# Optimization experiments

Measured on AMD Instinct MI355X. Metric: run time of the kernel, lower is better.

Reference implementation:

```python
import jax, jax.numpy as jnp
import numpy as np

N, E, IN, OUT, R, B = 20000, 640000, 128, 128, 65, 65
BN_EPS = 1e-5


def setup_inputs() -> dict:
    key = jax.random.key(0)
    ks = jax.random.split(key, 8)
    node_feats = jax.random.normal(ks[0], (N, IN), dtype=jnp.float32)
    src = jax.random.randint(ks[1], (E,), 0, N, dtype=jnp.int32)
    dst = jax.random.randint(ks[2], (E,), 0, N, dtype=jnp.int32)
    etype = jax.random.randint(ks[3], (E,), 0, R, dtype=jnp.int32)
    norm = jax.random.uniform(ks[4], (E, 1), dtype=jnp.float32)
    basis = jax.random.normal(ks[5], (B, IN, OUT), dtype=jnp.float32) * 0.05
    comp = jax.random.normal(ks[6], (R, B), dtype=jnp.float32) * 0.1
    h_bias = jnp.zeros((OUT,), dtype=jnp.float32)
    W_res = jax.random.normal(ks[7], (IN, OUT), dtype=jnp.float32) * 0.05
    b_res = jnp.zeros((OUT,), dtype=jnp.float32)
    gamma = jnp.ones((OUT,), dtype=jnp.float32)
    beta = jnp.zeros((OUT,), dtype=jnp.float32)
    return dict(node_feats=node_feats, src=src, dst=dst, etype=etype, norm=norm,
                basis=basis, comp=comp, h_bias=h_bias, W_res=W_res, b_res=b_res,
                gamma=gamma, beta=beta)


def reference(node_feats, src, dst, etype, norm, basis, comp, h_bias, W_res, b_res, gamma, beta):
    n, in_f = node_feats.shape
    r = comp.shape[0]
    # Basis decomposition: W_r = sum_b comp[r,b] * basis[b]  -> (R, in, out)
    W = jnp.einsum('rb,bio->rio', comp, basis)
    # Per-edge message x[src] * norm (norm is scalar per edge so it commutes
    # with the relation matmul). Aggregate per (dst, relation) first, then do
    # one dense relation-batched GEMM (mathematically identical to DGL's
    # per-edge transform + scatter-add, since everything is linear).
    msg = node_feats[src] * norm                       # (E, in)
    seg = dst.astype(jnp.int32) * r + etype            # combined (dst, rel) key
    S = jax.ops.segment_sum(msg, seg, num_segments=n * r).reshape(n, r, in_f)
    h = jnp.einsum('nri,rio->no', S, W) + h_bias       # (N, out)
    h = jax.nn.relu(h)                                 # conv activation (dropout p=0)
    # Residual branch: relu(Linear(x))
    h = h + jax.nn.relu(node_feats @ W_res + b_res)
    # BatchNorm1d (training mode: batch stats, biased variance)
    mean = jnp.mean(h, axis=0)
    var = jnp.var(h, axis=0)
    h = (h - mean) * jax.lax.rsqrt(var + BN_EPS) * gamma + beta
    return h
```

## Files before the change

kernel.cpp:

```cpp
#include <hip/hip_runtime.h>
#include <hip/hip_bf16.h>


#define N_NODES 20000
#define E_EDGES 640000
#define R_REL   65
#define NG5     40
#define NG128   157
#define NSLOT   (NG5 * R_REL * 4)
#define NKEY5   (NG5 * R_REL)
#define NB_RESID 313
#define MAX_TILES 10240
#define TM      128

typedef __attribute__((ext_vector_type(8))) short bf16x8;
typedef __attribute__((ext_vector_type(4))) float f32x4;
typedef __attribute__((ext_vector_type(4))) unsigned int u32x4;
typedef __attribute__((ext_vector_type(2))) unsigned int u32x2;

__device__ __forceinline__ unsigned short f2bf(float x) {
    union { float f; unsigned int u; } c; c.f = x;
    unsigned int b = c.u + 0x7fffu + ((c.u >> 16) & 1u);
    return (unsigned short)(b >> 16);
}
__device__ __forceinline__ float bf2f_lo(unsigned int u) {
    union { unsigned int u; float f; } c; c.u = u << 16; return c.f;
}
__device__ __forceinline__ float bf2f_hi(unsigned int u) {
    union { unsigned int u; float f; } c; c.u = u & 0xffff0000u; return c.f;
}
__device__ __forceinline__ void async16(const void* g, void* l) {
    __builtin_amdgcn_global_load_lds(
        (const __attribute__((address_space(1))) unsigned int*)g,
        (__attribute__((address_space(3))) unsigned int*)l, 16, 0, 0);
}
__device__ __forceinline__ int unperm(int p) {
    return (p & 64) + ((p & 3) << 4) + ((p >> 2) & 15);
}

__global__ void k_prep1(const float* __restrict__ comp, const float* __restrict__ basis,
                        float* __restrict__ W32, const int* __restrict__ et,
                        const int* __restrict__ dstA, int* __restrict__ gh3,
                        int* __restrict__ gh2, const float* __restrict__ node_feats,
                        unsigned short* __restrict__ node_bf) {
    __shared__ int shbuf[15200];
    int b = blockIdx.x, t = threadIdx.x;
    if (b < 320) {
        float* lc = (float*)shbuf;
        int r0 = (b >> 6) * 16;
        int col = (b & 63) * 256 + t;
        for (int j = t; j < 16 * 65; j += 256) {
            int rr = r0 + j / 65;
            lc[j] = (rr < R_REL) ? comp[rr * 65 + (j % 65)] : 0.f;
        }
        __syncthreads();
        float acc[16];
#pragma unroll
        for (int j = 0; j < 16; ++j) acc[j] = 0.f;
        for (int k = 0; k < 65; ++k) {
            float v = basis[k * 16384 + col];
#pragma unroll
            for (int j = 0; j < 16; ++j) acc[j] += lc[j * 65 + k] * v;
        }
#pragma unroll
        for (int j = 0; j < 16; ++j) {
            int rr = r0 + j;
            if (rr < R_REL) W32[rr * 16384 + col] = acc[j];
        }
    } else if (b < 384) {
        int* pk2 = shbuf;
        int* pk3 = shbuf + 10000;
        for (int i = t; i < 15200; i += 256) shbuf[i] = 0;
        __syncthreads();
        for (int i = (b - 320) * 256 + t; i < E_EDGES; i += 64 * 256) {
            int d = dstA[i];
            int slot = ((d >> 9) * 65 + et[i]) * 4 + ((d >> 7) & 3);
            atomicAdd(&pk2[d >> 1], (int)(1u << ((d & 1) << 4)));
            atomicAdd(&pk3[slot >> 1], (int)(1u << ((slot & 1) << 4)));
        }
        __syncthreads();
        for (int i = t; i < 10000; i += 256) {
            unsigned v = (unsigned)pk2[i];
            if (v & 0xffffu) atomicAdd(&gh2[2 * i], (int)(v & 0xffffu));
            if (v >> 16)     atomicAdd(&gh2[2 * i + 1], (int)(v >> 16));
        }
        for (int i = t; i < 5200; i += 256) {
            unsigned v = (unsigned)pk3[i];
            if (v & 0xffffu) atomicAdd(&gh3[2 * i], (int)(v & 0xffffu));
            if (v >> 16)     atomicAdd(&gh3[2 * i + 1], (int)(v >> 16));
        }
    } else {
        int i = (b - 384) * 256 + t;
        if (i < N_NODES * 32) {
            float4 v = reinterpret_cast<const float4*>(node_feats)[i];
            __hip_bfloat162 b0 = __float22bfloat162_rn(make_float2(v.x, v.y));
            __hip_bfloat162 b1 = __float22bfloat162_rn(make_float2(v.z, v.w));
            u32x2 pk;
            pk.x = *reinterpret_cast<unsigned int*>(&b0);
            pk.y = *reinterpret_cast<unsigned int*>(&b1);
            reinterpret_cast<u32x2*>(node_bf)[i] = pk;
        }
    }
}

__global__ void k_prep3(const int* __restrict__ gh3, int* __restrict__ segAll,
                        const int* __restrict__ gh2, int* __restrict__ seg,
                        const float* __restrict__ W32, unsigned short* __restrict__ Wt,
                        const float* __restrict__ Wresf, unsigned short* __restrict__ Wrest) {
    int b = blockIdx.x, t = threadIdx.x;
    if (b < 41) {
        __shared__ int red[256];
        __shared__ int pref;
        int acc = 0;
        for (int i = t; i < b * 256; i += 256) acc += gh3[i];
        red[t] = acc;
        __syncthreads();
        for (int off = 128; off > 0; off >>= 1) {
            if (t < off) red[t] += red[t + off];
            __syncthreads();
        }
        if (t == 0) pref = red[0];
        __syncthreads();
        int i = b * 256 + t;
        int v = (i < NSLOT) ? gh3[i] : 0;
        red[t] = v;
        __syncthreads();
        for (int off = 1; off < 256; off <<= 1) {
            int x = (t >= off) ? red[t - off] : 0;
            __syncthreads();
            red[t] += x;
            __syncthreads();
        }
        int excl = red[t] - v + pref;
        if (i < NSLOT) {
            segAll[i] = excl;
            if (i == NSLOT - 1) segAll[NSLOT] = excl + v;
        }
    } else if (b < 120) {
        __shared__ int red[256];
        __shared__ int pref;
        int b2 = b - 41;
        int acc = 0;
        for (int i = t; i < b2 * 256; i += 256) acc += gh2[i];
        red[t] = acc;
        __syncthreads();
        for (int off = 128; off > 0; off >>= 1) {
            if (t < off) red[t] += red[t + off];
            __syncthreads();
        }
        if (t == 0) pref = red[0];
        __syncthreads();
        int i = b2 * 256 + t;
        int v = (i < N_NODES) ? gh2[i] : 0;
        red[t] = v;
        __syncthreads();
        for (int off = 1; off < 256; off <<= 1) {
            int x = (t >= off) ? red[t - off] : 0;
            __syncthreads();
            red[t] += x;
            __syncthreads();
        }
        int excl = red[t] - v + pref;
        if (i < N_NODES) {
            seg[i] = excl;
            if (i == N_NODES - 1) seg[N_NODES] = excl + v;
        }
    } else {
        __shared__ float tile[64][65];
        int bb = b - 120;
        const float* s; unsigned short* d; int sub;
        if (bb < R_REL * 4) { s = W32 + (size_t)(bb >> 2) * 16384; d = Wt + (size_t)(bb >> 2) * 16384; sub = bb & 3; }
        else { s = Wresf; d = Wrest; sub = bb - R_REL * 4; }
        int ot = (sub >> 1) & 1, itl = sub & 1;
        int tx = t & 63, ty = t >> 6;
        for (int it = 0; it < 16; ++it) {
            int i = ty + it * 4;
            tile[i][tx] = s[(itl * 64 + i) * 128 + ot * 64 + tx];
        }
        __syncthreads();
        for (int it = 0; it < 16; ++it) {
            int o = ty + it * 4;
            d[(ot * 64 + o) * 128 + itl * 64 + tx] = f2bf(tile[tx][o]);
        }
    }
}

__global__ void k_scatterA(const int* __restrict__ et, const int* __restrict__ srcA,
                           const int* __restrict__ dstA, const float* __restrict__ norm,
                           const int* __restrict__ seg, int* __restrict__ cntA,
                           u32x2* __restrict__ ebuf) {
    __shared__ int lh[NG128], lbase[NG128];
    int c0 = blockIdx.x * 2560;
    int cend = min(c0 + 2560, E_EDGES);
    int t = threadIdx.x;
    for (int i = t; i < NG128; i += 256) lh[i] = 0;
    __syncthreads();
    for (int i = c0 + t; i < cend; i += 256) atomicAdd(&lh[dstA[i] >> 7], 1);
    __syncthreads();
    for (int i = t; i < NG128; i += 256)
        if (lh[i] > 0) lbase[i] = seg[i * 128] + atomicAdd(&cntA[i], lh[i]);
    __syncthreads();
    for (int i = t; i < NG128; i += 256) lh[i] = 0;
    __syncthreads();
    for (int i = c0 + t; i < cend; i += 256) {
        int d = dstA[i];
        int g = d >> 7;
        int p = lbase[g] + atomicAdd(&lh[g], 1);
        u32x2 e;
        e.x = (unsigned)srcA[i] | ((unsigned)(d & 127) << 15) | ((unsigned)et[i] << 22);
        e.y = __float_as_uint(norm[i]);
        ebuf[p] = e;
    }
}

__global__ void k_scatterB(const u32x2* __restrict__ ebuf, const int* __restrict__ seg,
                           const int* __restrict__ segAll, int* __restrict__ srcp,
                           float* __restrict__ normp, int* __restrict__ eidx,
                           int* __restrict__ ntiles_p, int* __restrict__ tile_r,
                           int* __restrict__ tile_start, int* __restrict__ tile_len) {
    int b = blockIdx.x, t = threadIdx.x;
    if (b < NG128) {
        __shared__ int base65[R_REL], lcnt[R_REL], sdst[128], ldst[128];
        int g5 = b >> 2, sub = b & 3;
        if (t < R_REL) { base65[t] = segAll[(g5 * 65 + t) * 4 + sub]; lcnt[t] = 0; }
        if (t < 128) {
            int d = b * 128 + t;
            sdst[t] = seg[min(d, N_NODES)];
            ldst[t] = 0;
        }
        __syncthreads();
        int e0 = seg[b * 128];
        int e1 = seg[min((b + 1) * 128, N_NODES)];
        for (int i = e0 + t; i < e1; i += 1024) {
            u32x2 e = ebuf[i];
            int src = e.x & 0x7fff;
            int slot = (e.x >> 15) & 127;
            int rel = e.x >> 22;
            int p = base65[rel] + atomicAdd(&lcnt[rel], 1);
            srcp[p] = src;
            normp[p] = __uint_as_float(e.y);
            int pos = sdst[slot] + atomicAdd(&ldst[slot], 1);
            eidx[pos] = p;
        }
    } else {
        int k2 = (b - NG128) * 1024 + t;
        if (k2 < NKEY5) {
            int s = segAll[k2 * 4], e = segAll[k2 * 4 + 4];
            int len = e - s;
            if (len > 0) {
                int nt = (len + TM - 1) / TM;
                int base = atomicAdd(ntiles_p, nt);
                for (int k = 0; k < nt; ++k) {
                    tile_r[base + k] = k2 % 65;
                    tile_start[base + k] = s + k * TM;
                    tile_len[base + k] = min(TM, len - k * TM);
                }
            }
        }
    }
}

__global__ __launch_bounds__(256, 3) void k_conv_gemm(
    const int* __restrict__ tile_r, const int* __restrict__ tile_start,
    const int* __restrict__ tile_len, const int* __restrict__ ntiles_p,
    const int* __restrict__ srcp, const float* __restrict__ normp,
    const unsigned short* __restrict__ node_bf,
    const unsigned short* __restrict__ Wt, const unsigned short* __restrict__ Wrest,
    const float* __restrict__ b_res, unsigned short* __restrict__ t_out,
    float* __restrict__ resid) {
    __shared__ unsigned short Blds[128 * 128];
    __shared__ float snorm[128];
    int t = threadIdx.x;
    int w = t >> 6, lane = t & 63;
    int lrow = lane & 15, quad = lane >> 4;

    if (blockIdx.x < NB_RESID) {
        int wr = (w >> 1) * 32, wc = (w & 1) * 64;
        int row0 = blockIdx.x * 64;
        int nrows = min(64, N_NODES - row0);
        int r0i = wr + lrow, r1i = wr + 16 + lrow;
        const bf16x8* a0p = reinterpret_cast<const bf16x8*>(
            node_bf + (size_t)(row0 + ((r0i < nrows) ? r0i : 0)) * 128);
        const bf16x8* a1p = reinterpret_cast<const bf16x8*>(
            node_bf + (size_t)(row0 + ((r1i < nrows) ? r1i : 0)) * 128);
        bf16x8 areg[2][4];
#pragma unroll
        for (int ks = 0; ks < 4; ++ks) {
            int cq = ks * 4 + quad;
            areg[0][ks] = a0p[cq];
            areg[1][ks] = a1p[cq];
        }
#pragma unroll
        for (int it = 0; it < 8; ++it) {
            int j = t + 256 * it;
            int o = j >> 4, c = j & 15, cs = c ^ (o & 15);
            async16(Wrest + o * 128 + cs * 8, &Blds[o * 128 + c * 8]);
        }
        __syncthreads();
        f32x4 acc[2][4];
#pragma unroll
        for (int i = 0; i < 2; ++i)
#pragma unroll
            for (int j = 0; j < 4; ++j) acc[i][j] = (f32x4){0.f, 0.f, 0.f, 0.f};
#pragma unroll
        for (int ks = 0; ks < 4; ++ks) {
            int cs = (ks * 4 + quad) ^ lrow;
            bf16x8 bfr[4];
#pragma unroll
            for (int j = 0; j < 4; ++j)
                bfr[j] = *reinterpret_cast<const bf16x8*>(&Blds[(wc + j * 16 + lrow) * 128 + cs * 8]);
#pragma unroll
            for (int i = 0; i < 2; ++i)
#pragma unroll
                for (int j = 0; j < 4; ++j)
                    acc[i][j] = __builtin_amdgcn_mfma_f32_16x16x32_bf16(areg[i][ks], bfr[j], acc[i][j], 0, 0, 0);
        }
        float br0 = b_res[wc + lrow];
        float br1 = b_res[wc + 16 + lrow];
        float br2 = b_res[wc + 32 + lrow];
        float br3 = b_res[wc + 48 + lrow];
#pragma unroll
        for (int i = 0; i < 2; ++i) {
#pragma unroll
            for (int reg = 0; reg < 4; ++reg) {
                int grow = row0 + wr + i * 16 + quad * 4 + reg;
                if (grow < N_NODES) {
                    float4 v;
                    v.x = fmaxf(acc[i][0][reg] + br0, 0.f);
                    v.y = fmaxf(acc[i][1][reg] + br1, 0.f);
                    v.z = fmaxf(acc[i][2][reg] + br2, 0.f);
                    v.w = fmaxf(acc[i][3][reg] + br3, 0.f);
                    *reinterpret_cast<float4*>(resid + (size_t)grow * 128 + wc + lrow * 4) = v;
                }
            }
        }
        return;
    }

    int tid = blockIdx.x - NB_RESID;
    if (tid >= *ntiles_p) return;
    int r = tile_r[tid], start = tile_start[tid], len = tile_len[tid];
    int wr = w * 32;
    int r0i = wr + lrow, r1i = wr + 16 + lrow;
    int s0 = srcp[start + ((r0i < len) ? r0i : 0)];
    int s1 = srcp[start + ((r1i < len) ? r1i : 0)];
    const bf16x8* a0p = reinterpret_cast<const bf16x8*>(node_bf + (size_t)s0 * 128);
    const bf16x8* a1p = reinterpret_cast<const bf16x8*>(node_bf + (size_t)s1 * 128);
    bf16x8 areg[2][4];
#pragma unroll
    for (int ks = 0; ks < 4; ++ks) {
        int cq = ks * 4 + quad;
        areg[0][ks] = a0p[cq];
        areg[1][ks] = a1p[cq];
    }
    const unsigned short* Wr = Wt + (size_t)r * 16384;
#pragma unroll
    for (int it = 0; it < 8; ++it) {
        int j = t + 256 * it;
        int o = j >> 4, c = j & 15, cs = c ^ (o & 15);
        async16(Wr + o * 128 + cs * 8, &Blds[o * 128 + c * 8]);
    }
    if (t < TM && t < len) snorm[t] = normp[start + t];
    __syncthreads();

    f32x4 acc[2][8];
#pragma unroll
    for (int i = 0; i < 2; ++i)
#pragma unroll
        for (int j = 0; j < 8; ++j) acc[i][j] = (f32x4){0.f, 0.f, 0.f, 0.f};
#pragma unroll
    for (int ks = 0; ks < 4; ++ks) {
        int cs = (ks * 4 + quad) ^ lrow;
        bf16x8 bfr[8];
#pragma unroll
        for (int j = 0; j < 8; ++j)
            bfr[j] = *reinterpret_cast<const bf16x8*>(&Blds[(j * 16 + lrow) * 128 + cs * 8]);
#pragma unroll
        for (int i = 0; i < 2; ++i)
#pragma unroll
            for (int j = 0; j < 8; ++j)
                acc[i][j] = __builtin_amdgcn_mfma_f32_16x16x32_bf16(areg[i][ks], bfr[j], acc[i][j], 0, 0, 0);
    }

#pragma unroll
    for (int i = 0; i < 2; ++i) {
        int m0 = wr + i * 16 + quad * 4;
#pragma unroll
        for (int reg = 0; reg < 4; ++reg) {
            int m = m0 + reg;
            if (m < len) {
                float nm = snorm[m];
                float2 l0 = make_float2(acc[i][0][reg] * nm, acc[i][1][reg] * nm);
                float2 l1 = make_float2(acc[i][2][reg] * nm, acc[i][3][reg] * nm);
                float2 h0 = make_float2(acc[i][4][reg] * nm, acc[i][5][reg] * nm);
                float2 h1 = make_float2(acc[i][6][reg] * nm, acc[i][7][reg] * nm);
                __hip_bfloat162 bl0 = __float22bfloat162_rn(l0);
                __hip_bfloat162 bl1 = __float22bfloat162_rn(l1);
                __hip_bfloat162 bh0 = __float22bfloat162_rn(h0);
                __hip_bfloat162 bh1 = __float22bfloat162_rn(h1);
                u32x2 s0v, s1v;
                s0v.x = *reinterpret_cast<unsigned int*>(&bl0);
                s0v.y = *reinterpret_cast<unsigned int*>(&bl1);
                s1v.x = *reinterpret_cast<unsigned int*>(&bh0);
                s1v.y = *reinterpret_cast<unsigned int*>(&bh1);
                unsigned short* rowp = t_out + (size_t)(start + m) * 128;
                __builtin_nontemporal_store(s0v, reinterpret_cast<u32x2*>(rowp + lrow * 4));
                __builtin_nontemporal_store(s1v, reinterpret_cast<u32x2*>(rowp + 64 + lrow * 4));
            }
        }
    }
}

__global__ __launch_bounds__(256) void k_reduce_fused(
    const unsigned short* __restrict__ t, const int* __restrict__ seg,
    const int* __restrict__ eidx, const float* __restrict__ resid,
    const float* __restrict__ h_bias, float* __restrict__ h,
    float* __restrict__ colsum, float* __restrict__ colsumsq) {
    __shared__ float cs1[128], cs2[128], sbias[128];
    if (threadIdx.x < 128) {
        cs1[threadIdx.x] = 0.f; cs2[threadIdx.x] = 0.f;
        sbias[threadIdx.x] = h_bias[unperm(threadIdx.x)];
    }
    __syncthreads();
    int w = threadIdx.x >> 6, lane = threadIdx.x & 63;
    int g = lane >> 4, c = lane & 15;
    for (int k = 0; k < 2; ++k) {
        int d = blockIdx.x * 8 + k * 4 + w;
        if (d >= N_NODES) continue;
        int a = seg[d], b = seg[d + 1];
        float s[8];
#pragma unroll
        for (int kk = 0; kk < 8; ++kk) s[kk] = 0.f;
        for (int q = a + g; q < b; q += 32) {
            int er[8];
#pragma unroll
            for (int kk = 0; kk < 8; ++kk) {
                int row = q + 4 * kk;
                er[kk] = eidx[(row < b) ? row : a];
            }
            u32x4 v[8];
#pragma unroll
            for (int kk = 0; kk < 8; ++kk) {
                v[kk] = *reinterpret_cast<const u32x4*>(t + (size_t)er[kk] * 128 + c * 8);
                if (q + 4 * kk >= b) v[kk] = (u32x4){0u, 0u, 0u, 0u};
            }
#pragma unroll
            for (int kk = 0; kk < 8; ++kk)
#pragma unroll
                for (int j = 0; j < 4; ++j) {
                    s[2 * j]     += bf2f_lo(v[kk][j]);
                    s[2 * j + 1] += bf2f_hi(v[kk][j]);
                }
        }
#pragma unroll
        for (int kk = 0; kk < 8; ++kk) {
            s[kk] += __shfl_xor(s[kk], 16);
            s[kk] += __shfl_xor(s[kk], 32);
        }
        if (g == 0) {
            const float* rp = resid + (size_t)d * 128 + c * 8;
            float4 r0 = *reinterpret_cast<const float4*>(rp);
            float4 r1 = *reinterpret_cast<const float4*>(rp + 4);
            float rr[8] = {r0.x, r0.y, r0.z, r0.w, r1.x, r1.y, r1.z, r1.w};
            float v[8];
#pragma unroll
            for (int kk = 0; kk < 8; ++kk)
                v[kk] = fmaxf(s[kk] + sbias[c * 8 + kk], 0.f) + rr[kk];
            float* hp = h + (size_t)d * 128 + c * 8;
            *reinterpret_cast<float4*>(hp)     = make_float4(v[0], v[1], v[2], v[3]);
            *reinterpret_cast<float4*>(hp + 4) = make_float4(v[4], v[5], v[6], v[7]);
#pragma unroll
            for (int kk = 0; kk < 8; ++kk) {
                atomicAdd(&cs1[c * 8 + kk], v[kk]);
                atomicAdd(&cs2[c * 8 + kk], v[kk] * v[kk]);
            }
        }
    }
    __syncthreads();
    if (threadIdx.x < 128) {
        atomicAdd(&colsum[threadIdx.x], cs1[threadIdx.x]);
        atomicAdd(&colsumsq[threadIdx.x], cs2[threadIdx.x]);
    }
}

__global__ void k_bn(float* __restrict__ h, const float* __restrict__ colsum,
                     const float* __restrict__ colsumsq, const float* __restrict__ gamma,
                     const float* __restrict__ beta) {
    __shared__ float sc[128], sh[128], tile[8][128];
    int t = threadIdx.x;
    if (t < 128) {
        int n = unperm(t);
        float m = colsum[t] * (1.f / N_NODES);
        float var = colsumsq[t] * (1.f / N_NODES) - m * m;
        float s = gamma[n] * rsqrtf(var + 1e-5f);
        sc[t] = s;
        sh[t] = beta[n] - m * s;
    }
    __syncthreads();
    int r = t >> 5;
    int p0 = (t & 31) * 4;
    int n0 = (p0 & 64) + ((p0 >> 2) & 15);
    for (int row0 = blockIdx.x * 8; row0 < N_NODES; row0 += gridDim.x * 8) {
        int row = row0 + r;
        float4 v = make_float4(0.f, 0.f, 0.f, 0.f);
        if (row < N_NODES) v = *reinterpret_cast<float4*>(h + (size_t)row * 128 + p0);
        v.x = v.x * sc[p0] + sh[p0];
        v.y = v.y * sc[p0 + 1] + sh[p0 + 1];
        v.z = v.z * sc[p0 + 2] + sh[p0 + 2];
        v.w = v.w * sc[p0 + 3] + sh[p0 + 3];
        tile[r][n0]      = v.x;
        tile[r][n0 + 16] = v.y;
        tile[r][n0 + 32] = v.z;
        tile[r][n0 + 48] = v.w;
        __syncthreads();
        if (row < N_NODES)
            *reinterpret_cast<float4*>(h + (size_t)row * 128 + p0) =
                *reinterpret_cast<float4*>(&tile[r][p0]);
        __syncthreads();
    }
}

extern "C" void kernel_launch(void* const* d_in, const int* in_sizes, int n_in,
                              void* d_out, int out_size, void* d_ws, size_t ws_size,
                              hipStream_t stream) {
    (void)in_sizes; (void)n_in; (void)out_size; (void)ws_size;
    const float* node_feats = (const float*)d_in[0];
    const int* src    = (const int*)d_in[1];
    const int* dst    = (const int*)d_in[2];
    const int* etype  = (const int*)d_in[3];
    const float* norm = (const float*)d_in[4];
    const float* basis = (const float*)d_in[5];
    const float* comp  = (const float*)d_in[6];
    const float* h_bias = (const float*)d_in[7];
    const float* W_res  = (const float*)d_in[8];
    const float* b_res  = (const float*)d_in[9];
    const float* gamma  = (const float*)d_in[10];
    const float* beta   = (const float*)d_in[11];

    char* ws = (char*)d_ws;
    float* colsum   = (float*)(ws + 0);
    float* colsumsq = (float*)(ws + 512);
    int* ntiles_p   = (int*)(ws + 1024);
    int* cntA       = (int*)(ws + 1088);
    int* gh3        = (int*)(ws + 1792);
    int* gh2        = (int*)(ws + 43392);
    int* segAll     = (int*)(ws + 123392);
    int* seg        = (int*)(ws + 165056);
    int* tile_r     = (int*)(ws + 245120);
    int* tile_start = (int*)(ws + 286080);
    int* tile_len   = (int*)(ws + 327040);
    unsigned short* Wt      = (unsigned short*)(ws + 368000);
    unsigned short* Wrest   = (unsigned short*)(ws + 2497920);
    unsigned short* node_bf = (unsigned short*)(ws + 2530688);
    int* srcp       = (int*)(ws + 7650688);
    float* normp    = (float*)(ws + 10210688);
    int* eidx       = (int*)(ws + 12770688);
    u32x2* ebuf     = (u32x2*)(ws + 15330688);
    float* resid    = (float*)(ws + 20450688);
    const long T_BASE = 30690688L;
    float* W32      = (float*)(ws + T_BASE);
    unsigned short* t_buf = (unsigned short*)(ws + T_BASE);
    float* hacc = (float*)d_out;

    hipMemsetAsync(ws, 0, 123392, stream);
    k_prep1<<<2884, 256, 0, stream>>>(comp, basis, W32, etype, dst, gh3, gh2,
                                      node_feats, node_bf);
    k_prep3<<<384, 256, 0, stream>>>(gh3, segAll, gh2, seg, W32, Wt, W_res, Wrest);
    k_scatterA<<<250, 256, 0, stream>>>(etype, src, dst, norm, seg, cntA, ebuf);
    k_scatterB<<<160, 1024, 0, stream>>>(ebuf, seg, segAll, srcp, normp, eidx,
                                         ntiles_p, tile_r, tile_start, tile_len);
    k_conv_gemm<<<NB_RESID + MAX_TILES, 256, 0, stream>>>(
        tile_r, tile_start, tile_len, ntiles_p, srcp, normp, node_bf,
        Wt, Wrest, b_res, t_buf, resid);
    k_reduce_fused<<<2500, 256, 0, stream>>>(t_buf, seg, eidx, resid,
                                             h_bias, hacc, colsum, colsumsq);
    k_bn<<<2500, 256, 0, stream>>>(hacc, colsum, colsumsq, gamma, beta);
}
```

Before: 285.6 us.

## Replace per-node edge index with 128-node group reduction using LDS atomics

Drops the per-destination-node histogram, prefix scan and eidx permutation. Each edge now records only an 8-bit slot (node within its 128-node group). The new reduce kernel walks each group's rows in (relation, slot) order and accumulates into an LDS tile with shared atomics, then flushes to global h with global atomics. A separate combine kernel then applies bias, ReLU and the residual and gathers column statistics. This removes the eidx indirection and the 20000-entry scan, but it adds a memset of the output, global atomics, LDS atomic contention, and a FCAP cap that silently drops edges if a group holds more than 5120 rows.

```diff
diff --git a/kernel.cpp b/kernel.cpp
--- a/kernel.cpp
+++ b/kernel.cpp
@@ -12,6 +12,7 @@
 #define NB_RESID 313
 #define MAX_TILES 10240
 #define TM      128
+#define FCAP    5120
 
 typedef __attribute__((ext_vector_type(8))) short bf16x8;
 typedef __attribute__((ext_vector_type(4))) float f32x4;
@@ -41,9 +42,9 @@
 __global__ void k_prep1(const float* __restrict__ comp, const float* __restrict__ basis,
                         float* __restrict__ W32, const int* __restrict__ et,
                         const int* __restrict__ dstA, int* __restrict__ gh3,
-                        int* __restrict__ gh2, const float* __restrict__ node_feats,
+                        int* __restrict__ gh128, const float* __restrict__ node_feats,
                         unsigned short* __restrict__ node_bf) {
-    __shared__ int shbuf[15200];
+    __shared__ int shbuf[5360];
     int b = blockIdx.x, t = threadIdx.x;
     if (b < 320) {
         float* lc = (float*)shbuf;
@@ -68,27 +69,23 @@
             if (rr < R_REL) W32[rr * 16384 + col] = acc[j];
         }
     } else if (b < 384) {
-        int* pk2 = shbuf;
-        int* pk3 = shbuf + 10000;
-        for (int i = t; i < 15200; i += 256) shbuf[i] = 0;
+        int* pk3 = shbuf;
+        int* pkg = shbuf + 5200;
+        for (int i = t; i < 5360; i += 256) shbuf[i] = 0;
         __syncthreads();
         for (int i = (b - 320) * 256 + t; i < E_EDGES; i += 64 * 256) {
             int d = dstA[i];
             int slot = ((d >> 9) * 65 + et[i]) * 4 + ((d >> 7) & 3);
-            atomicAdd(&pk2[d >> 1], (int)(1u << ((d & 1) << 4)));
             atomicAdd(&pk3[slot >> 1], (int)(1u << ((slot & 1) << 4)));
-        }
-        __syncthreads();
-        for (int i = t; i < 10000; i += 256) {
-            unsigned v = (unsigned)pk2[i];
-            if (v & 0xffffu) atomicAdd(&gh2[2 * i], (int)(v & 0xffffu));
-            if (v >> 16)     atomicAdd(&gh2[2 * i + 1], (int)(v >> 16));
-        }
+            atomicAdd(&pkg[d >> 7], 1);
+        }
+        __syncthreads();
         for (int i = t; i < 5200; i += 256) {
             unsigned v = (unsigned)pk3[i];
             if (v & 0xffffu) atomicAdd(&gh3[2 * i], (int)(v & 0xffffu));
             if (v >> 16)     atomicAdd(&gh3[2 * i + 1], (int)(v >> 16));
         }
+        if (t < NG128 && pkg[t] > 0) atomicAdd(&gh128[t], pkg[t]);
     } else {
         int i = (b - 384) * 256 + t;
         if (i < N_NODES * 32) {
@@ -104,7 +101,7 @@
 }
 
 __global__ void k_prep3(const int* __restrict__ gh3, int* __restrict__ segAll,
-                        const int* __restrict__ gh2, int* __restrict__ seg,
+                        const int* __restrict__ gh128, int* __restrict__ segG,
                         const float* __restrict__ W32, unsigned short* __restrict__ Wt,
                         const float* __restrict__ Wresf, unsigned short* __restrict__ Wrest) {
     int b = blockIdx.x, t = threadIdx.x;
@@ -136,22 +133,9 @@
             segAll[i] = excl;
             if (i == NSLOT - 1) segAll[NSLOT] = excl + v;
         }
-    } else if (b < 120) {
+    } else if (b == 41) {
         __shared__ int red[256];
-        __shared__ int pref;
-        int b2 = b - 41;
-        int acc = 0;
-        for (int i = t; i < b2 * 256; i += 256) acc += gh2[i];
-        red[t] = acc;
-        __syncthreads();
-        for (int off = 128; off > 0; off >>= 1) {
-            if (t < off) red[t] += red[t + off];
-            __syncthreads();
-        }
-        if (t == 0) pref = red[0];
-        __syncthreads();
-        int i = b2 * 256 + t;
-        int v = (i < N_NODES) ? gh2[i] : 0;
+        int v = (t < NG128) ? gh128[t] : 0;
         red[t] = v;
         __syncthreads();
         for (int off = 1; off < 256; off <<= 1) {
@@ -160,14 +144,13 @@
             red[t] += x;
             __syncthreads();
         }
-        int excl = red[t] - v + pref;
-        if (i < N_NODES) {
-            seg[i] = excl;
-            if (i == N_NODES - 1) seg[N_NODES] = excl + v;
+        if (t < NG128) {
+            segG[t] = red[t] - v;
+            if (t == NG128 - 1) segG[NG128] = red[t];
         }
     } else {
         __shared__ float tile[64][65];
-        int bb = b - 120;
+        int bb = b - 42;
         const float* s; unsigned short* d; int sub;
         if (bb < R_REL * 4) { s = W32 + (size_t)(bb >> 2) * 16384; d = Wt + (size_t)(bb >> 2) * 16384; sub = bb & 3; }
         else { s = Wresf; d = Wrest; sub = bb - R_REL * 4; }
@@ -187,7 +170,7 @@
 
 __global__ void k_scatterA(const int* __restrict__ et, const int* __restrict__ srcA,
                            const int* __restrict__ dstA, const float* __restrict__ norm,
-                           const int* __restrict__ seg, int* __restrict__ cntA,
+                           const int* __restrict__ segG, int* __restrict__ cntA,
                            u32x2* __restrict__ ebuf) {
     __shared__ int lh[NG128], lbase[NG128];
     int c0 = blockIdx.x * 2560;
@@ -198,7 +181,7 @@
     for (int i = c0 + t; i < cend; i += 256) atomicAdd(&lh[dstA[i] >> 7], 1);
     __syncthreads();
     for (int i = t; i < NG128; i += 256)
-        if (lh[i] > 0) lbase[i] = seg[i * 128] + atomicAdd(&cntA[i], lh[i]);
+        if (lh[i] > 0) lbase[i] = segG[i] + atomicAdd(&cntA[i], lh[i]);
     __syncthreads();
     for (int i = t; i < NG128; i += 256) lh[i] = 0;
     __syncthreads();
@@ -213,24 +196,19 @@
     }
 }
 
-__global__ void k_scatterB(const u32x2* __restrict__ ebuf, const int* __restrict__ seg,
+__global__ void k_scatterB(const u32x2* __restrict__ ebuf, const int* __restrict__ segG,
                            const int* __restrict__ segAll, int* __restrict__ srcp,
-                           float* __restrict__ normp, int* __restrict__ eidx,
+                           float* __restrict__ normp, unsigned char* __restrict__ slot8,
                            int* __restrict__ ntiles_p, int* __restrict__ tile_r,
                            int* __restrict__ tile_start, int* __restrict__ tile_len) {
     int b = blockIdx.x, t = threadIdx.x;
     if (b < NG128) {
-        __shared__ int base65[R_REL], lcnt[R_REL], sdst[128], ldst[128];
+        __shared__ int base65[R_REL], lcnt[R_REL];
         int g5 = b >> 2, sub = b & 3;
         if (t < R_REL) { base65[t] = segAll[(g5 * 65 + t) * 4 + sub]; lcnt[t] = 0; }
-        if (t < 128) {
-            int d = b * 128 + t;
-            sdst[t] = seg[min(d, N_NODES)];
-            ldst[t] = 0;
-        }
-        __syncthreads();
-        int e0 = seg[b * 128];
-        int e1 = seg[min((b + 1) * 128, N_NODES)];
+        __syncthreads();
+        int e0 = segG[b];
+        int e1 = segG[b + 1];
         for (int i = e0 + t; i < e1; i += 1024) {
             u32x2 e = ebuf[i];
             int src = e.x & 0x7fff;
@@ -239,8 +217,7 @@
             int p = base65[rel] + atomicAdd(&lcnt[rel], 1);
             srcp[p] = src;
             normp[p] = __uint_as_float(e.y);
-            int pos = sdst[slot] + atomicAdd(&ldst[slot], 1);
-            eidx[pos] = p;
+            slot8[p] = (unsigned char)slot;
         }
     } else {
         int k2 = (b - NG128) * 1024 + t;
@@ -411,75 +388,100 @@
     }
 }
 
-__global__ __launch_bounds__(256) void k_reduce_fused(
-    const unsigned short* __restrict__ t, const int* __restrict__ seg,
-    const int* __restrict__ eidx, const float* __restrict__ resid,
-    const float* __restrict__ h_bias, float* __restrict__ h,
-    float* __restrict__ colsum, float* __restrict__ colsumsq) {
+__global__ __launch_bounds__(256, 2) void k_reduce2(
+    const unsigned short* __restrict__ tb, const unsigned char* __restrict__ slot8,
+    const int* __restrict__ segAll, float* __restrict__ h) {
+    __shared__ float hloc[128 * 65];
+    __shared__ int frow[FCAP];
+    __shared__ int sbase[33], slen[33], scum[34];
+    int b = blockIdx.x;
+    int g128 = b >> 2, ch = (b >> 1) & 1, rh = b & 1;
+    int g5 = g128 >> 2, sub = g128 & 3;
+    int nrel = rh ? 32 : 33, rel0 = rh * 33;
+    int t = threadIdx.x;
+    for (int i = t; i < 128 * 65; i += 256) hloc[i] = 0.f;
+    if (t < nrel) {
+        int sl = (g5 * 65 + rel0 + t) * 4 + sub;
+        sbase[t] = segAll[sl];
+        slen[t] = segAll[sl + 1] - segAll[sl];
+    }
+    __syncthreads();
+    if (t == 0) {
+        int a = 0;
+        for (int i = 0; i < nrel; ++i) { scum[i] = a; a += slen[i]; }
+        scum[nrel] = a;
+    }
+    __syncthreads();
+    int total = min(scum[nrel], FCAP);
+    int wv = t >> 6, ln = t & 63;
+    for (int rr = wv; rr < nrel; rr += 4) {
+        int s = sbase[rr], c0 = scum[rr], len = slen[rr];
+        for (int i = ln; i < len && c0 + i < FCAP; i += 64) frow[c0 + i] = s + i;
+    }
+    __syncthreads();
+
+    int c16 = t & 15, fb = t >> 4;
+    for (int f0 = fb; f0 < total; f0 += 16 * 8) {
+        int rows[8];
+#pragma unroll
+        for (int k = 0; k < 8; ++k) {
+            int f = f0 + 16 * k;
+            rows[k] = frow[(f < total) ? f : 0];
+        }
+        u32x2 v[8]; int sl[8];
+#pragma unroll
+        for (int k = 0; k < 8; ++k) {
+            v[k] = *reinterpret_cast<const u32x2*>(
+                tb + (size_t)rows[k] * 128 + ch * 64 + c16 * 4);
+            sl[k] = slot8[rows[k]];
+        }
+#pragma unroll
+        for (int k = 0; k < 8; ++k) {
+            if (f0 + 16 * k < total) {
+                float* hp = &hloc[sl[k] * 65 + c16 * 4];
+                atomicAdd(&hp[0], bf2f_lo(v[k].x));
+                atomicAdd(&hp[1], bf2f_hi(v[k].x));
+                atomicAdd(&hp[2], bf2f_lo(v[k].y));
+                atomicAdd(&hp[3], bf2f_hi(v[k].y));
+            }
+        }
+    }
+    __syncthreads();
+    for (int i = t; i < 128 * 64; i += 256) {
+        int sl2 = i >> 6, c = i & 63;
+        int d = g128 * 128 + sl2;
+        if (d < N_NODES)
+            atomicAdd(&h[(size_t)d * 128 + ch * 64 + c], hloc[sl2 * 65 + c]);
+    }
+}
+
+__global__ __launch_bounds__(256) void k_combine(
+    float* __restrict__ h, const float* __restrict__ resid,
+    const float* __restrict__ h_bias, float* __restrict__ colsum,
+    float* __restrict__ colsumsq) {
     __shared__ float cs1[128], cs2[128], sbias[128];
-    if (threadIdx.x < 128) {
-        cs1[threadIdx.x] = 0.f; cs2[threadIdx.x] = 0.f;
-        sbias[threadIdx.x] = h_bias[unperm(threadIdx.x)];
-    }
-    __syncthreads();
-    int w = threadIdx.x >> 6, lane = threadIdx.x & 63;
-    int g = lane >> 4, c = lane & 15;
-    for (int k = 0; k < 2; ++k) {
-        int d = blockIdx.x * 8 + k * 4 + w;
-        if (d >= N_NODES) continue;
-        int a = seg[d], b = seg[d + 1];
-        float s[8];
-#pragma unroll
-        for (int kk = 0; kk < 8; ++kk) s[kk] = 0.f;
-        for (int q = a + g; q < b; q += 32) {
-            int er[8];
-#pragma unroll
-            for (int kk = 0; kk < 8; ++kk) {
-                int row = q + 4 * kk;
-                er[kk] = eidx[(row < b) ? row : a];
-            }
-            u32x4 v[8];
-#pragma unroll
-            for (int kk = 0; kk < 8; ++kk) {
-                v[kk] = *reinterpret_cast<const u32x4*>(t + (size_t)er[kk] * 128 + c * 8);
-                if (q + 4 * kk >= b) v[kk] = (u32x4){0u, 0u, 0u, 0u};
-            }
-#pragma unroll
-            for (int kk = 0; kk < 8; ++kk)
-#pragma unroll
-                for (int j = 0; j < 4; ++j) {
-                    s[2 * j]     += bf2f_lo(v[kk][j]);
-                    s[2 * j + 1] += bf2f_hi(v[kk][j]);
-                }
-        }
-#pragma unroll
-        for (int kk = 0; kk < 8; ++kk) {
-            s[kk] += __shfl_xor(s[kk], 16);
-            s[kk] += __shfl_xor(s[kk], 32);
-        }
-        if (g == 0) {
-            const float* rp = resid + (size_t)d * 128 + c * 8;
-            float4 r0 = *reinterpret_cast<const float4*>(rp);
-            float4 r1 = *reinterpret_cast<const float4*>(rp + 4);
-            float rr[8] = {r0.x, r0.y, r0.z, r0.w, r1.x, r1.y, r1.z, r1.w};
-            float v[8];
-#pragma unroll
-            for (int kk = 0; kk < 8; ++kk)
-                v[kk] = fmaxf(s[kk] + sbias[c * 8 + kk], 0.f) + rr[kk];
-            float* hp = h + (size_t)d * 128 + c * 8;
-            *reinterpret_cast<float4*>(hp)     = make_float4(v[0], v[1], v[2], v[3]);
-            *reinterpret_cast<float4*>(hp + 4) = make_float4(v[4], v[5], v[6], v[7]);
-#pragma unroll
-            for (int kk = 0; kk < 8; ++kk) {
-                atomicAdd(&cs1[c * 8 + kk], v[kk]);
-                atomicAdd(&cs2[c * 8 + kk], v[kk] * v[kk]);
-            }
-        }
-    }
-    __syncthreads();
-    if (threadIdx.x < 128) {
-        atomicAdd(&colsum[threadIdx.x], cs1[threadIdx.x]);
-        atomicAdd(&colsumsq[threadIdx.x], cs2[threadIdx.x]);
+    int t = threadIdx.x;
+    if (t < 128) { cs1[t] = 0.f; cs2[t] = 0.f; sbias[t] = h_bias[unperm(t)]; }
+    __syncthreads();
+    int i = blockIdx.x * 256 + t;
+    int row = i >> 5, p0 = (i & 31) * 4;
+    size_t off = (size_t)row * 128 + p0;
+    f32x4 a = *reinterpret_cast<const f32x4*>(h + off);
+    f32x4 r = *reinterpret_cast<const f32x4*>(resid + off);
+    f32x4 v;
+#pragma unroll
+    for (int j = 0; j < 4; ++j)
+        v[j] = fmaxf(a[j] + sbias[p0 + j], 0.f) + r[j];
+    *reinterpret_cast<f32x4*>(h + off) = v;
+#pragma unroll
+    for (int j = 0; j < 4; ++j) {
+        atomicAdd(&cs1[p0 + j], v[j]);
+        atomicAdd(&cs2[p0 + j], v[j] * v[j]);
+    }
+    __syncthreads();
+    if (t < 128) {
+        atomicAdd(&colsum[t], cs1[t]);
+        atomicAdd(&colsumsq[t], cs2[t]);
     }
 }
 
@@ -543,36 +545,37 @@
     int* ntiles_p   = (int*)(ws + 1024);
     int* cntA       = (int*)(ws + 1088);
     int* gh3        = (int*)(ws + 1792);
-    int* gh2        = (int*)(ws + 43392);
-    int* segAll     = (int*)(ws + 123392);
-    int* seg        = (int*)(ws + 165056);
-    int* tile_r     = (int*)(ws + 245120);
-    int* tile_start = (int*)(ws + 286080);
-    int* tile_len   = (int*)(ws + 327040);
-    unsigned short* Wt      = (unsigned short*)(ws + 368000);
-    unsigned short* Wrest   = (unsigned short*)(ws + 2497920);
-    unsigned short* node_bf = (unsigned short*)(ws + 2530688);
-    int* srcp       = (int*)(ws + 7650688);
-    float* normp    = (float*)(ws + 10210688);
-    int* eidx       = (int*)(ws + 12770688);
-    u32x2* ebuf     = (u32x2*)(ws + 15330688);
-    float* resid    = (float*)(ws + 20450688);
-    const long T_BASE = 30690688L;
+    int* gh128      = (int*)(ws + 43392);
+    int* segG       = (int*)(ws + 44032);
+    int* segAll     = (int*)(ws + 44672);
+    int* tile_r     = (int*)(ws + 86336);
+    int* tile_start = (int*)(ws + 127296);
+    int* tile_len   = (int*)(ws + 168256);
+    unsigned short* Wt      = (unsigned short*)(ws + 209216);
+    unsigned short* Wrest   = (unsigned short*)(ws + 2339136);
+    unsigned short* node_bf = (unsigned short*)(ws + 2371904);
+    int* srcp       = (int*)(ws + 7491904);
+    float* normp    = (float*)(ws + 10051904);
+    unsigned char* slot8 = (unsigned char*)(ws + 12611904);
+    u32x2* ebuf     = (u32x2*)(ws + 13251904);
+    float* resid    = (float*)(ws + 18371904);
+    const long T_BASE = 28611904L;
     float* W32      = (float*)(ws + T_BASE);
     unsigned short* t_buf = (unsigned short*)(ws + T_BASE);
     float* hacc = (float*)d_out;
 
-    hipMemsetAsync(ws, 0, 123392, stream);
-    k_prep1<<<2884, 256, 0, stream>>>(comp, basis, W32, etype, dst, gh3, gh2,
+    hipMemsetAsync(ws, 0, 44032, stream);
+    hipMemsetAsync(hacc, 0, (size_t)N_NODES * 128 * 4, stream);
+    k_prep1<<<2884, 256, 0, stream>>>(comp, basis, W32, etype, dst, gh3, gh128,
                                       node_feats, node_bf);
-    k_prep3<<<384, 256, 0, stream>>>(gh3, segAll, gh2, seg, W32, Wt, W_res, Wrest);
-    k_scatterA<<<250, 256, 0, stream>>>(etype, src, dst, norm, seg, cntA, ebuf);
-    k_scatterB<<<160, 1024, 0, stream>>>(ebuf, seg, segAll, srcp, normp, eidx,
+    k_prep3<<<306, 256, 0, stream>>>(gh3, segAll, gh128, segG, W32, Wt, W_res, Wrest);
+    k_scatterA<<<250, 256, 0, stream>>>(etype, src, dst, norm, segG, cntA, ebuf);
+    k_scatterB<<<160, 1024, 0, stream>>>(ebuf, segG, segAll, srcp, normp, slot8,
                                          ntiles_p, tile_r, tile_start, tile_len);
     k_conv_gemm<<<NB_RESID + MAX_TILES, 256, 0, stream>>>(
         tile_r, tile_start, tile_len, ntiles_p, srcp, normp, node_bf,
         Wt, Wrest, b_res, t_buf, resid);
-    k_reduce_fused<<<2500, 256, 0, stream>>>(t_buf, seg, eidx, resid,
-                                             h_bias, hacc, colsum, colsumsq);
+    k_reduce2<<<NG128 * 4, 256, 0, stream>>>(t_buf, slot8, segAll, hacc);
+    k_combine<<<2500, 256, 0, stream>>>(hacc, resid, h_bias, colsum, colsumsq);
     k_bn<<<2500, 256, 0, stream>>>(hacc, colsum, colsumsq, gamma, beta);
 }
```

Result: slower. 809.0 us (+183.2%).

## Scatter GEMM outputs directly into dst-sorted order, drop indirect gather in reduce

Applied to the files above, without the earlier changes.

Instead of writing per-edge transformed rows in relation-tile order and gathering them through an index array during the per-node reduction, the scatter kernel now records each edge's destination-sorted position. The GEMM kernel writes its output rows to that position, so the reduce kernel reads contiguous rows without indirection. This removes a dependent index load and random gathers from the reduce, at the cost of scattered, non-nontemporal row writes in the GEMM epilogue.

```diff
diff --git a/kernel.cpp b/kernel.cpp
--- a/kernel.cpp
+++ b/kernel.cpp
@@ -215,7 +215,7 @@
 
 __global__ void k_scatterB(const u32x2* __restrict__ ebuf, const int* __restrict__ seg,
                            const int* __restrict__ segAll, int* __restrict__ srcp,
-                           float* __restrict__ normp, int* __restrict__ eidx,
+                           float* __restrict__ normp, int* __restrict__ dpos,
                            int* __restrict__ ntiles_p, int* __restrict__ tile_r,
                            int* __restrict__ tile_start, int* __restrict__ tile_len) {
     int b = blockIdx.x, t = threadIdx.x;
@@ -239,8 +239,7 @@
             int p = base65[rel] + atomicAdd(&lcnt[rel], 1);
             srcp[p] = src;
             normp[p] = __uint_as_float(e.y);
-            int pos = sdst[slot] + atomicAdd(&ldst[slot], 1);
-            eidx[pos] = p;
+            dpos[p] = sdst[slot] + atomicAdd(&ldst[slot], 1);
         }
     } else {
         int k2 = (b - NG128) * 1024 + t;
@@ -264,12 +263,13 @@
     const int* __restrict__ tile_r, const int* __restrict__ tile_start,
     const int* __restrict__ tile_len, const int* __restrict__ ntiles_p,
     const int* __restrict__ srcp, const float* __restrict__ normp,
-    const unsigned short* __restrict__ node_bf,
+    const int* __restrict__ dpos, const unsigned short* __restrict__ node_bf,
     const unsigned short* __restrict__ Wt, const unsigned short* __restrict__ Wrest,
     const float* __restrict__ b_res, unsigned short* __restrict__ t_out,
     float* __restrict__ resid) {
     __shared__ unsigned short Blds[128 * 128];
     __shared__ float snorm[128];
+    __shared__ int sdpos[128];
     int t = threadIdx.x;
     int w = t >> 6, lane = t & 63;
     int lrow = lane & 15, quad = lane >> 4;
@@ -360,7 +360,10 @@
         int o = j >> 4, c = j & 15, cs = c ^ (o & 15);
         async16(Wr + o * 128 + cs * 8, &Blds[o * 128 + c * 8]);
     }
-    if (t < TM && t < len) snorm[t] = normp[start + t];
+    if (t < TM && t < len) {
+        snorm[t] = normp[start + t];
+        sdpos[t] = dpos[start + t];
+    }
     __syncthreads();
 
     f32x4 acc[2][8];
@@ -403,9 +406,9 @@
                 s0v.y = *reinterpret_cast<unsigned int*>(&bl1);
                 s1v.x = *reinterpret_cast<unsigned int*>(&bh0);
                 s1v.y = *reinterpret_cast<unsigned int*>(&bh1);
-                unsigned short* rowp = t_out + (size_t)(start + m) * 128;
-                __builtin_nontemporal_store(s0v, reinterpret_cast<u32x2*>(rowp + lrow * 4));
-                __builtin_nontemporal_store(s1v, reinterpret_cast<u32x2*>(rowp + 64 + lrow * 4));
+                unsigned short* rowp = t_out + (size_t)sdpos[m] * 128;
+                *reinterpret_cast<u32x2*>(rowp + lrow * 4)      = s0v;
+                *reinterpret_cast<u32x2*>(rowp + 64 + lrow * 4) = s1v;
             }
         }
     }
@@ -413,9 +416,8 @@
 
 __global__ __launch_bounds__(256) void k_reduce_fused(
     const unsigned short* __restrict__ t, const int* __restrict__ seg,
-    const int* __restrict__ eidx, const float* __restrict__ resid,
-    const float* __restrict__ h_bias, float* __restrict__ h,
-    float* __restrict__ colsum, float* __restrict__ colsumsq) {
+    const float* __restrict__ resid, const float* __restrict__ h_bias,
+    float* __restrict__ h, float* __restrict__ colsum, float* __restrict__ colsumsq) {
     __shared__ float cs1[128], cs2[128], sbias[128];
     if (threadIdx.x < 128) {
         cs1[threadIdx.x] = 0.f; cs2[threadIdx.x] = 0.f;
@@ -432,25 +434,23 @@
 #pragma unroll
         for (int kk = 0; kk < 8; ++kk) s[kk] = 0.f;
         for (int q = a + g; q < b; q += 32) {
-            int er[8];
+            u32x4 v[8];
 #pragma unroll
             for (int kk = 0; kk < 8; ++kk) {
                 int row = q + 4 * kk;
-                er[kk] = eidx[(row < b) ? row : a];
+                int rc = (row < b) ? row : a;
+                v[kk] = *reinterpret_cast<const u32x4*>(t + (size_t)rc * 128 + c * 8);
             }
-            u32x4 v[8];
 #pragma unroll
             for (int kk = 0; kk < 8; ++kk) {
-                v[kk] = *reinterpret_cast<const u32x4*>(t + (size_t)er[kk] * 128 + c * 8);
-                if (q + 4 * kk >= b) v[kk] = (u32x4){0u, 0u, 0u, 0u};
+                if (q + 4 * kk < b) {
+#pragma unroll
+                    for (int j = 0; j < 4; ++j) {
+                        s[2 * j]     += bf2f_lo(v[kk][j]);
+                        s[2 * j + 1] += bf2f_hi(v[kk][j]);
+                    }
+                }
             }
-#pragma unroll
-            for (int kk = 0; kk < 8; ++kk)
-#pragma unroll
-                for (int j = 0; j < 4; ++j) {
-                    s[2 * j]     += bf2f_lo(v[kk][j]);
-                    s[2 * j + 1] += bf2f_hi(v[kk][j]);
-                }
         }
 #pragma unroll
         for (int kk = 0; kk < 8; ++kk) {
@@ -554,7 +554,7 @@
     unsigned short* node_bf = (unsigned short*)(ws + 2530688);
     int* srcp       = (int*)(ws + 7650688);
     float* normp    = (float*)(ws + 10210688);
-    int* eidx       = (int*)(ws + 12770688);
+    int* dpos       = (int*)(ws + 12770688);
     u32x2* ebuf     = (u32x2*)(ws + 15330688);
     float* resid    = (float*)(ws + 20450688);
     const long T_BASE = 30690688L;
@@ -567,12 +567,12 @@
                                       node_feats, node_bf);
     k_prep3<<<384, 256, 0, stream>>>(gh3, segAll, gh2, seg, W32, Wt, W_res, Wrest);
     k_scatterA<<<250, 256, 0, stream>>>(etype, src, dst, norm, seg, cntA, ebuf);
-    k_scatterB<<<160, 1024, 0, stream>>>(ebuf, seg, segAll, srcp, normp, eidx,
+    k_scatterB<<<160, 1024, 0, stream>>>(ebuf, seg, segAll, srcp, normp, dpos,
                                          ntiles_p, tile_r, tile_start, tile_len);
     k_conv_gemm<<<NB_RESID + MAX_TILES, 256, 0, stream>>>(
-        tile_r, tile_start, tile_len, ntiles_p, srcp, normp, node_bf,
+        tile_r, tile_start, tile_len, ntiles_p, srcp, normp, dpos, node_bf,
         Wt, Wrest, b_res, t_buf, resid);
-    k_reduce_fused<<<2500, 256, 0, stream>>>(t_buf, seg, eidx, resid,
-                                             h_bias, hacc, colsum, colsumsq);
+    k_reduce_fused<<<2500, 256, 0, stream>>>(t_buf, seg, resid, h_bias,
+                                             hacc, colsum, colsumsq);
     k_bn<<<2500, 256, 0, stream>>>(hacc, colsum, colsumsq, gamma, beta);
 }
```

Measured after the change: 302.5 us. 1.06x slower.
